# Performance work log

Measured on AMD Instinct MI355X. Metric: run time of the kernel, lower is better.

The kernel has to match this reference:

```python
import jax, jax.numpy as jnp
import numpy as np

HID = 192
EPS = 1e-5

def _bn(x, g, b):
    # BatchNorm1d, training mode: batch stats over all leading axes, biased var
    ax = tuple(range(x.ndim - 1))
    m = x.mean(axis=ax)
    v = x.var(axis=ax)
    return (x - m) * jax.lax.rsqrt(v + EPS) * g + b

def _glorot(k, shape):
    lim = np.sqrt(6.0 / (shape[0] + shape[1]))
    return jax.random.uniform(k, shape, jnp.float32, -lim, lim)

def setup_inputs() -> dict:
    key = jax.random.key(0)
    ks = jax.random.split(key, 8)
    B, N, F, C = 16, 1024, 128, 10
    x = jax.random.normal(ks[0], (B, N, F), jnp.float32)
    adj = (jax.random.uniform(ks[1], (B, N, N)) < 0.01).astype(jnp.float32)
    adj = jnp.maximum(adj, jnp.swapaxes(adj, 1, 2))
    return dict(
        x=x, adj=adj,
        bn_feat_g=jnp.ones((F,), jnp.float32), bn_feat_b=jnp.full((F,), 1e-4, jnp.float32),
        W_feat=_glorot(ks[2], (F, HID)),
        bns_conv_g=jnp.ones((3, HID), jnp.float32), bns_conv_b=jnp.full((3, HID), 1e-4, jnp.float32),
        convs_W=jnp.stack([_glorot(jax.random.fold_in(ks[3], i), (HID, HID)) for i in range(3)]),
        convs_b=jnp.zeros((3, HID), jnp.float32),
        bn_fc_g=jnp.ones((HID,), jnp.float32), bn_fc_b=jnp.full((HID,), 1e-4, jnp.float32),
        lin_W=_glorot(ks[4], (HID, HID)), lin_b=jnp.zeros((HID,), jnp.float32),
        bn_hid_g=jnp.ones((HID,), jnp.float32), bn_hid_b=jnp.full((HID,), 1e-4, jnp.float32),
        cls_W=_glorot(ks[5], (HID, 10)), cls_b=jnp.zeros((10,), jnp.float32),
    )

def reference(x, adj, bn_feat_g, bn_feat_b, W_feat, bns_conv_g, bns_conv_b,
              convs_W, convs_b, bn_fc_g, bn_fc_b, lin_W, lin_b,
              bn_hid_g, bn_hid_b, cls_W, cls_b):
    B, N, _ = x.shape
    # dense_to_sparse discards edge values -> binary edges; add remaining self loops (weight 1)
    A = (adj != 0).astype(x.dtype)
    A = jnp.maximum(A, jnp.eye(N, dtype=x.dtype))
    deg = A.sum(-1)                                   # [B,N]
    dis = jnp.where(deg > 0, deg ** -0.5, 0.0)
    A_hat = dis[:, :, None] * A * dis[:, None, :]      # D^-1/2 (A+I) D^-1/2
    h = _bn(x, bn_feat_g, bn_feat_b)
    # conv_feat has gfn=True: pure linear transform, no bias, no propagation
    h = jax.nn.relu(jnp.einsum('bnf,fh->bnh', h, W_feat))
    for i in range(convs_W.shape[0]):
        h = _bn(h, bns_conv_g[i], bns_conv_b[i])
        h = jax.nn.relu(jnp.einsum('bij,bjh->bih', A_hat, h @ convs_W[i]) + convs_b[i])
    g = h.mean(axis=1)                                 # global_mean_pool -> [B,HID]
    g = _bn(g, bn_fc_g, bn_fc_b)
    g = jax.nn.relu(g @ lin_W + lin_b)
    g = _bn(g, bn_hid_g, bn_hid_b)
    logits = g @ cls_W + cls_b
    return jax.nn.log_softmax(logits, axis=-1)
```

## Files before the change

### kernel.cpp

```cpp
#include <hip/hip_runtime.h>
#include <hip/hip_bf16.h>

#define BB 16
#define NN 1024
#define FF 128
#define HH 192
#define NROWS (BB*NN)
#define MAXC 128
#define EPSV 1e-5f

constexpr size_t OFF_H0  = 0;
constexpr size_t OFF_ZB  = OFF_H0 + (size_t)NROWS*HH/2;
constexpr size_t OFF_WPF = OFF_ZB + (size_t)NROWS*HH/2;
constexpr size_t OFF_WPC = OFF_WPF + (size_t)HH*FF/2;
constexpr size_t OFF_BF  = OFF_WPC + (size_t)HH*HH/2;
constexpr size_t OFF_BC  = OFF_BF + HH;
constexpr size_t OFF_DIS = OFF_BC + HH;
constexpr size_t OFF_G   = OFF_DIS + NROWS;
constexpr size_t OFF_ST  = OFF_G + BB*HH;
constexpr size_t ST_SIZE = 512 + 3*8*512;
constexpr size_t OFF_FLAG= OFF_ST + ST_SIZE;
constexpr size_t OFF_CNT = OFF_FLAG + 1;
constexpr size_t OFF_COLS= OFF_CNT + NROWS;

typedef __attribute__((ext_vector_type(8))) short short8;
typedef __attribute__((ext_vector_type(4))) float f32x4;
typedef __attribute__((ext_vector_type(4))) unsigned int u32x4;
typedef __attribute__((ext_vector_type(2))) unsigned int u32x2;

static __device__ __forceinline__ float bf(const __hip_bfloat16 v) {
    return __bfloat162float(v);
}
static __device__ __forceinline__ float ldin(const void* p, size_t i, int isf) {
    return isf ? ((const float*)p)[i]
               : __bfloat162float(((const __hip_bfloat16*)p)[i]);
}
static __host__ __device__ __forceinline__ float* stage_h(float* ws, int s ) {
    return ws + OFF_ST + 512 + (size_t)s*8*512;
}

__global__ void detect_and_zero(const unsigned int* __restrict__ adjw, float* ws) {
    __shared__ int evid;
    int tid = threadIdx.x;
    if (tid == 0) evid = 0;
    __syncthreads();
    int local = 0;
    for (int k = tid; k < 16384; k += 256) {
        unsigned int w = adjw[k];
        if ((w & 0xFFFFu) == 0x3F80u) local++;
    }
    if (local) atomicAdd(&evid, local);
    for (size_t k = tid; k < ST_SIZE; k += 256) ws[OFF_ST + k] = 0.f;
    for (int k = tid; k < BB*HH; k += 256) ws[OFF_G + k] = 0.f;
    __syncthreads();
    if (tid == 0) ((int*)ws)[OFF_FLAG] = (evid == 0) ? 1 : 0;
}

__global__ __launch_bounds__(256) void phase1(const void* __restrict__ adj,
                                              const void* __restrict__ x, float* ws) {
    const int isf = ((const int*)ws)[OFF_FLAG];
    int tid = threadIdx.x;
    if (blockIdx.x < NROWS) {
        int row = blockIdx.x;
        int i   = row & (NN - 1);
        __shared__ int cnt_s;
        __shared__ unsigned short colbuf[MAXC];
        if (tid == 0) cnt_s = 0;
        __syncthreads();
        int j0 = tid*4;
        unsigned int bits[4];
        if (isf) {
            u32x4 v = *(const u32x4*)((const unsigned int*)adj + (size_t)row*NN + j0);
            bits[0]=v[0]; bits[1]=v[1]; bits[2]=v[2]; bits[3]=v[3];
        } else {
            u32x2 v = *(const u32x2*)((const unsigned short*)adj + (size_t)row*NN + j0);
            bits[0]=(v[0]&0xFFFFu); bits[1]=(v[0]>>16); bits[2]=(v[1]&0xFFFFu); bits[3]=(v[1]>>16);
        }
        #pragma unroll
        for (int e = 0; e < 4; ++e) {
            int j = j0 + e;
            if ((bits[e] << 1) != 0u || j == i) {
                int p = atomicAdd(&cnt_s, 1);
                if (p < MAXC) colbuf[p] = (unsigned short)j;
            }
        }
        __syncthreads();
        int c = cnt_s; if (c > MAXC) c = MAXC;
        if (tid == 0) {
            ((int*)(ws + OFF_CNT))[row] = c;
            ws[OFF_DIS + row] = rsqrtf((float)cnt_s);
        }
        unsigned short* cols = (unsigned short*)(ws + OFF_COLS);
        for (int k = tid; k < c; k += 256) cols[(size_t)row*MAXC + k] = colbuf[k];
    } else {
        int b2 = blockIdx.x - NROWS;
        int f = tid & (FF-1), half = tid >> 7;
        int r0 = b2*64 + half*32;
        float s = 0.f, sq = 0.f;
        for (int r = 0; r < 32; ++r) {
            float v = ldin(x, (size_t)(r0 + r)*FF + f, isf);
            s += v; sq += v*v;
        }
        atomicAdd(&ws[OFF_ST + f], s);
        atomicAdd(&ws[OFF_ST + 256 + f], sq);
    }
}

__global__ void prep_feat(const void* __restrict__ W_feat,
                          const void* __restrict__ gg, const void* __restrict__ bb,
                          float* ws) {
    const int isf = ((const int*)ws)[OFF_FLAG];
    int n = blockIdx.x, k = threadIdx.x;
    const float* st = ws + OFF_ST;
    float m   = st[k] * (1.f/NROWS);
    float var = st[256+k] * (1.f/NROWS) - m*m;
    float a   = ldin(gg, k, isf) * rsqrtf(var + EPSV);
    float c   = ldin(bb, k, isf) - m*a;
    float wv  = ldin(W_feat, (size_t)k*HH + n, isf);
    ((__hip_bfloat16*)(ws + OFF_WPF))[(size_t)n*FF + k] = __float2bfloat16(a*wv);
    __shared__ float red[FF];
    red[k] = c*wv;
    __syncthreads();
    for (int s = FF/2; s > 0; s >>= 1) {
        if (k < s) red[k] += red[k + s];
        __syncthreads();
    }
    if (k == 0) ws[OFF_BF + n] = red[0];
}

__global__ void prep_conv(const void* __restrict__ convs_W,
                          const void* __restrict__ gg, const void* __restrict__ bb,
                          int layer, float* ws) {
    const int isf = ((const int*)ws)[OFF_FLAG];
    int n = blockIdx.x, k = threadIdx.x;
    const float* st = stage_h(ws, layer);
    float s = 0.f, sq = 0.f;
    #pragma unroll
    for (int bkt = 0; bkt < 8; ++bkt) {
        s  += st[bkt*512 + k];
        sq += st[bkt*512 + 256 + k];
    }
    float m   = s * (1.f/NROWS);
    float var = sq * (1.f/NROWS) - m*m;
    float a   = ldin(gg, (size_t)layer*HH + k, isf) * rsqrtf(var + EPSV);
    float c   = ldin(bb, (size_t)layer*HH + k, isf) - m*a;
    float wv  = ldin(convs_W, (size_t)layer*HH*HH + (size_t)k*HH + n, isf);
    ((__hip_bfloat16*)(ws + OFF_WPC))[(size_t)n*HH + k] = __float2bfloat16(a*wv);
    __shared__ float red[HH];
    red[k] = c*wv;
    __syncthreads();
    if (k < 96) red[k] += red[k + 96];
    __syncthreads();
    for (int s2 = 48; s2 >= 3; s2 >>= 1) {
        if (k < s2) red[k] += red[k + s2];
        __syncthreads();
    }
    if (k == 0) ws[OFF_BC + n] = red[0] + red[1] + red[2];
}

template<int K, int MODE>
__global__ __launch_bounds__(256) void gemm_mfma(const void* __restrict__ A,
                                                 const __hip_bfloat16* __restrict__ BT,
                                                 const float* __restrict__ bias,
                                                 float* __restrict__ ws) {
    const int isf = ((const int*)ws)[OFF_FLAG];
    int lane = threadIdx.x & 63, w = threadIdx.x >> 6;
    int wr = w & 1, wc = w >> 1;
    int row0 = blockIdx.x*32 + wr*16;
    int col0 = wc*96;
    int m    = lane & 15, quad = lane >> 4;
    f32x4 acc[6];
    #pragma unroll
    for (int t = 0; t < 6; ++t) acc[t] = f32x4{0.f,0.f,0.f,0.f};
    float bv[6];
    #pragma unroll
    for (int t = 0; t < 6; ++t) bv[t] = bias[col0 + t*16 + m];
    #pragma unroll
    for (int kb = 0; kb < K/32; ++kb) {
        short8 a;
        if (MODE == 0 && isf) {
            const float* Ar = (const float*)A + (size_t)(row0+m)*K + kb*32 + quad*8;
            f32x4 v0 = *(const f32x4*)Ar;
            f32x4 v1 = *(const f32x4*)(Ar + 4);
            union { short8 s8; __hip_bfloat16 h[8]; } u;
            #pragma unroll
            for (int e = 0; e < 4; ++e) {
                u.h[e]   = __float2bfloat16(v0[e]);
                u.h[e+4] = __float2bfloat16(v1[e]);
            }
            a = u.s8;
        } else {
            a = *(const short8*)((const __hip_bfloat16*)A +
                                 (size_t)(row0+m)*K + kb*32 + quad*8);
        }
        #pragma unroll
        for (int t = 0; t < 6; ++t) {
            short8 b = *(const short8*)(BT + (size_t)(col0 + t*16+m)*K + kb*32 + quad*8);
            acc[t] = __builtin_amdgcn_mfma_f32_16x16x32_bf16(a, b, acc[t], 0, 0, 0);
        }
    }
    if (MODE == 0) {
        __shared__ float sh[2*HH];
        for (int i = threadIdx.x; i < 2*HH; i += 256) sh[i] = 0.f;
        __syncthreads();
        __hip_bfloat16* H0 = (__hip_bfloat16*)(ws + OFF_H0);
        #pragma unroll
        for (int t = 0; t < 6; ++t) {
            int ch = col0 + t*16 + m;
            float s = 0.f, sq = 0.f;
            #pragma unroll
            for (int r = 0; r < 4; ++r) {
                float o = fmaxf(acc[t][r] + bv[t], 0.f);
                H0[(size_t)(row0 + quad*4 + r)*HH + ch] = __float2bfloat16(o);
                s += o; sq += o*o;
            }
            atomicAdd(&sh[ch], s);
            atomicAdd(&sh[HH + ch], sq);
        }
        __syncthreads();
        float* st = stage_h(ws, 0) + (blockIdx.x & 7)*512;
        if (threadIdx.x < HH) {
            atomicAdd(&st[threadIdx.x], sh[threadIdx.x]);
            atomicAdd(&st[256 + threadIdx.x], sh[HH + threadIdx.x]);
        }
    } else {
        const float* dis = ws + OFF_DIS;
        __hip_bfloat16* Z = (__hip_bfloat16*)(ws + OFF_ZB);
        float sc[4];
        #pragma unroll
        for (int r = 0; r < 4; ++r) sc[r] = dis[row0 + quad*4 + r];
        #pragma unroll
        for (int t = 0; t < 6; ++t)
            #pragma unroll
            for (int r = 0; r < 4; ++r)
                Z[(size_t)(row0 + quad*4 + r)*HH + col0 + t*16 + m] =
                    __float2bfloat16((acc[t][r] + bv[t]) * sc[r]);
    }
}

__global__ __launch_bounds__(192) void spmm(const void* __restrict__ bias, int layer,
                                            float* __restrict__ stat_out, int is_pool,
                                            float* ws) {
    int tid = threadIdx.x;
    const int isf = ((const int*)ws)[OFF_FLAG];
    const float* dis = ws + OFF_DIS;
    const int* cnt = (const int*)(ws + OFF_CNT);
    const unsigned short* cols = (const unsigned short*)(ws + OFF_COLS);
    const __hip_bfloat16* Z = (const __hip_bfloat16*)(ws + OFF_ZB);
    __hip_bfloat16* H0 = (__hip_bfloat16*)(ws + OFF_H0);
    int r0 = blockIdx.x * 4;
    int base = (r0 >> 10) << 10;
    float bl = ldin(bias, (size_t)layer*HH + tid, isf);
    float s = 0.f, sq = 0.f;
    #pragma unroll
    for (int rr = 0; rr < 4; ++rr) {
        int row = r0 + rr;
        int c = cnt[row];
        const unsigned short* cl = cols + (size_t)row*MAXC;
        float acc = 0.f;
        int k = 0;
        for (; k + 4 <= c; k += 4) {
            int j0 = base + cl[k],   j1 = base + cl[k+1];
            int j2 = base + cl[k+2], j3 = base + cl[k+3];
            acc += bf(Z[(size_t)j0*HH + tid]) + bf(Z[(size_t)j1*HH + tid])
                 + bf(Z[(size_t)j2*HH + tid]) + bf(Z[(size_t)j3*HH + tid]);
        }
        for (; k < c; ++k) acc += bf(Z[(size_t)(base + cl[k])*HH + tid]);
        float o = fmaxf(dis[row]*acc + bl, 0.f);
        H0[(size_t)row*HH + tid] = __float2bfloat16(o);
        s += o; sq += o*o;
    }
    if (is_pool) {
        atomicAdd(&ws[OFF_G + (size_t)(r0 >> 10)*HH + tid], s);
    } else {
        float* st = stat_out + (blockIdx.x & 7)*512;
        atomicAdd(&st[tid], s);
        atomicAdd(&st[256 + tid], sq);
    }
}

__global__ __launch_bounds__(768) void tail(
                     const void* __restrict__ fc_g,  const void* __restrict__ fc_b,
                     const void* __restrict__ lin_W, const void* __restrict__ lin_b,
                     const void* __restrict__ hid_g, const void* __restrict__ hid_b,
                     const void* __restrict__ cls_W, const void* __restrict__ cls_b,
                     void* __restrict__ out, const float* ws) {
    __shared__ float g1[BB][HH];
    __shared__ float g2[BB][HH];
    __shared__ __hip_bfloat16 Wl[HH*HH];
    __shared__ float logits[BB][10];
    __shared__ float lse[BB];
    int tid = threadIdx.x;
    const int isf = ((const int*)ws)[OFF_FLAG];
    const float* g = ws + OFF_G;
    if (isf) {
        const float* Wp = (const float*)lin_W;
        for (int i = tid; i < HH*HH; i += 768) Wl[i] = __float2bfloat16(Wp[i]);
    } else {
        const __hip_bfloat16* Wp = (const __hip_bfloat16*)lin_W;
        for (int i = tid; i < HH*HH; i += 768) Wl[i] = Wp[i];
    }
    if (tid < HH) {
        float s = 0.f, sq = 0.f;
        for (int b = 0; b < BB; ++b) {
            float v = g[b*HH + tid] * (1.f/NN);
            s += v; sq += v*v;
        }
        float m = s*(1.f/BB), var = sq*(1.f/BB) - m*m;
        float a = ldin(fc_g, tid, isf) * rsqrtf(var + EPSV);
        float c = ldin(fc_b, tid, isf) - m*a;
        for (int b = 0; b < BB; ++b) g1[b][tid] = g[b*HH + tid]*(1.f/NN)*a + c;
    }
    __syncthreads();
    {
        int n = tid % HH, bg = tid / HH;
        float lb = ldin(lin_b, n, isf);
        float a0 = lb, a1 = lb, a2 = lb, a3 = lb;
        int b0 = bg*4;
        for (int k = 0; k < HH; ++k) {
            float wv = bf(Wl[k*HH + n]);
            a0 += g1[b0+0][k]*wv;
            a1 += g1[b0+1][k]*wv;
            a2 += g1[b0+2][k]*wv;
            a3 += g1[b0+3][k]*wv;
        }
        g2[b0+0][n] = fmaxf(a0, 0.f);
        g2[b0+1][n] = fmaxf(a1, 0.f);
        g2[b0+2][n] = fmaxf(a2, 0.f);
        g2[b0+3][n] = fmaxf(a3, 0.f);
    }
    __syncthreads();
    if (tid < HH) {
        float s = 0.f, sq = 0.f;
        for (int b = 0; b < BB; ++b) { float v = g2[b][tid]; s += v; sq += v*v; }
        float m = s*(1.f/BB), var = sq*(1.f/BB) - m*m;
        float a = ldin(hid_g, tid, isf) * rsqrtf(var + EPSV);
        float c = ldin(hid_b, tid, isf) - m*a;
        for (int b = 0; b < BB; ++b) g2[b][tid] = g2[b][tid]*a + c;
    }
    __syncthreads();
    if (tid < BB*10) {
        int b = tid/10, k = tid%10;
        float acc = ldin(cls_b, k, isf);
        for (int h = 0; h < HH; ++h) acc += g2[b][h] * ldin(cls_W, (size_t)h*10 + k, isf);
        logits[b][k] = acc;
    }
    __syncthreads();
    if (tid < BB) {
        float m = -1e30f;
        for (int k = 0; k < 10; ++k) m = fmaxf(m, logits[tid][k]);
        float s = 0.f;
        for (int k = 0; k < 10; ++k) s += expf(logits[tid][k] - m);
        lse[tid] = m + logf(s);
    }
    __syncthreads();
    if (tid < BB*10) {
        int b = tid/10;
        float v = logits[b][tid%10] - lse[b];
        if (isf) ((float*)out)[tid] = v;
        else     ((__hip_bfloat16*)out)[tid] = __float2bfloat16(v);
    }
}

extern "C" void kernel_launch(void* const* d_in, const int* in_sizes, int n_in,
                              void* d_out, int out_size, void* d_ws, size_t ws_size,
                              hipStream_t stream) {
    const void* x       = d_in[0];
    const void* adj     = d_in[1];
    const void* bnf_g   = d_in[2];
    const void* bnf_b   = d_in[3];
    const void* W_feat  = d_in[4];
    const void* bnc_g   = d_in[5];
    const void* bnc_b   = d_in[6];
    const void* convs_W = d_in[7];
    const void* convs_b = d_in[8];
    const void* fc_g    = d_in[9];
    const void* fc_b    = d_in[10];
    const void* lin_W   = d_in[11];
    const void* lin_b   = d_in[12];
    const void* hid_g   = d_in[13];
    const void* hid_b   = d_in[14];
    const void* cls_W   = d_in[15];
    const void* cls_b   = d_in[16];

    float* ws = (float*)d_ws;
    const __hip_bfloat16* WPF = (const __hip_bfloat16*)(ws + OFF_WPF);
    const __hip_bfloat16* WPC = (const __hip_bfloat16*)(ws + OFF_WPC);

    detect_and_zero<<<1, 256, 0, stream>>>((const unsigned int*)adj, ws);
    phase1<<<NROWS + 256, 256, 0, stream>>>(adj, x, ws);
    prep_feat<<<HH, FF, 0, stream>>>(W_feat, bnf_g, bnf_b, ws);
    gemm_mfma<FF, 0><<<NROWS/32, 256, 0, stream>>>(x, WPF, ws + OFF_BF, ws);
    for (int l = 0; l < 3; ++l) {
        prep_conv<<<HH, HH, 0, stream>>>(convs_W, bnc_g, bnc_b, l, ws);
        gemm_mfma<HH, 1><<<NROWS/32, 256, 0, stream>>>(
            (const void*)(ws + OFF_H0), WPC, ws + OFF_BC, ws);
        spmm<<<NROWS/4, HH, 0, stream>>>(convs_b, l,
            (l < 2) ? stage_h(ws, l + 1) : nullptr, (l == 2) ? 1 : 0, ws);
    }
    tail<<<1, 768, 0, stream>>>(fc_g, fc_b, lin_W, lin_b,
                                hid_g, hid_b, cls_W, cls_b, d_out, ws);
}
```

Before: 387.1 us.

## Restructure SpMM to process rows in parallel with packed bf16 loads

The SpMM kernel now assigns 96 threads per row, with each thread loading two packed bf16 channels as one 32-bit word. Four rows are handled concurrently per block instead of sequentially. Column indices are read eight at a time with a vector load, and per-block statistics are reduced through shared-memory atomics before the global atomics. Block indices in both the GEMM and SpMM kernels are interleaved across batches so that concurrently running blocks touch different graphs. This trades sequential per-row loops for more memory-level parallelism, at the cost of a block-wide sync and extra shared atomics.

```diff
diff --git a/kernel.cpp b/kernel.cpp
--- a/kernel.cpp
+++ b/kernel.cpp
@@ -38,6 +38,17 @@
 static __host__ __device__ __forceinline__ float* stage_h(float* ws, int s ) {
     return ws + OFF_ST + 512 + (size_t)s*8*512;
 }
+static __device__ __forceinline__ float blo(unsigned int u) {
+    union { unsigned int x; float f; } v; v.x = u << 16; return v.f;
+}
+static __device__ __forceinline__ float bhi(unsigned int u) {
+    union { unsigned int x; float f; } v; v.x = u & 0xFFFF0000u; return v.f;
+}
+static __device__ __forceinline__ unsigned int packbf(float a, float b) {
+    union { unsigned int u; __hip_bfloat16 h[2]; } p;
+    p.h[0] = __float2bfloat16(a); p.h[1] = __float2bfloat16(b);
+    return p.u;
+}
 
 __global__ void detect_and_zero(const unsigned int* __restrict__ adjw, float* ws) {
     __shared__ int evid;
@@ -166,7 +177,9 @@
     const int isf = ((const int*)ws)[OFF_FLAG];
     int lane = threadIdx.x & 63, w = threadIdx.x >> 6;
     int wr = w & 1, wc = w >> 1;
-    int row0 = blockIdx.x*32 + wr*16;
+    int bi = blockIdx.x;
+    int batch = bi & 15, seg = bi >> 4;
+    int row0 = batch*NN + seg*32 + wr*16;
     int col0 = wc*96;
     int m    = lane & 15, quad = lane >> 4;
     f32x4 acc[6];
@@ -218,7 +231,7 @@
             atomicAdd(&sh[HH + ch], sq);
         }
         __syncthreads();
-        float* st = stage_h(ws, 0) + (blockIdx.x & 7)*512;
+        float* st = stage_h(ws, 0) + (bi & 7)*512;
         if (threadIdx.x < HH) {
             atomicAdd(&st[threadIdx.x], sh[threadIdx.x]);
             atomicAdd(&st[256 + threadIdx.x], sh[HH + threadIdx.x]);
@@ -238,44 +251,71 @@
     }
 }
 
-__global__ __launch_bounds__(192) void spmm(const void* __restrict__ bias, int layer,
+__global__ __launch_bounds__(384) void spmm(const void* __restrict__ bias, int layer,
                                             float* __restrict__ stat_out, int is_pool,
                                             float* ws) {
     int tid = threadIdx.x;
-    const int isf = ((const int*)ws)[OFF_FLAG];
+    int rl  = tid / 96;
+    int t   = tid - rl*96;
+    const int isf = ((const int*)ws)[OFF_FLAG];
+    int bi = blockIdx.x;
+    int batch = bi & 15, seg = bi >> 4;
+    int row  = batch*NN + seg*4 + rl;
+    int base = batch*NN;
     const float* dis = ws + OFF_DIS;
-    const int* cnt = (const int*)(ws + OFF_CNT);
-    const unsigned short* cols = (const unsigned short*)(ws + OFF_COLS);
-    const __hip_bfloat16* Z = (const __hip_bfloat16*)(ws + OFF_ZB);
-    __hip_bfloat16* H0 = (__hip_bfloat16*)(ws + OFF_H0);
-    int r0 = blockIdx.x * 4;
-    int base = (r0 >> 10) << 10;
-    float bl = ldin(bias, (size_t)layer*HH + tid, isf);
-    float s = 0.f, sq = 0.f;
-    #pragma unroll
-    for (int rr = 0; rr < 4; ++rr) {
-        int row = r0 + rr;
-        int c = cnt[row];
-        const unsigned short* cl = cols + (size_t)row*MAXC;
-        float acc = 0.f;
-        int k = 0;
-        for (; k + 4 <= c; k += 4) {
-            int j0 = base + cl[k],   j1 = base + cl[k+1];
-            int j2 = base + cl[k+2], j3 = base + cl[k+3];
-            acc += bf(Z[(size_t)j0*HH + tid]) + bf(Z[(size_t)j1*HH + tid])
-                 + bf(Z[(size_t)j2*HH + tid]) + bf(Z[(size_t)j3*HH + tid]);
-        }
-        for (; k < c; ++k) acc += bf(Z[(size_t)(base + cl[k])*HH + tid]);
-        float o = fmaxf(dis[row]*acc + bl, 0.f);
-        H0[(size_t)row*HH + tid] = __float2bfloat16(o);
-        s += o; sq += o*o;
-    }
+    int c = ((const int*)(ws + OFF_CNT))[row];
+    const unsigned short* cl = (const unsigned short*)(ws + OFF_COLS) + (size_t)row*MAXC;
+    const unsigned int* Zu = (const unsigned int*)(ws + OFF_ZB);
+    __shared__ float sh_s[HH];
+    __shared__ float sh_q[HH];
+    if (!is_pool) {
+        for (int i = tid; i < HH; i += 384) { sh_s[i] = 0.f; sh_q[i] = 0.f; }
+    } else {
+        for (int i = tid; i < HH; i += 384) sh_s[i] = 0.f;
+    }
+    __syncthreads();
+    float a0 = 0.f, a1 = 0.f;
+    int k = 0;
+    for (; k + 8 <= c; k += 8) {
+        u32x4 cw = *(const u32x4*)(cl + k);
+        int j[8];
+        j[0] = (int)(cw[0] & 0xFFFFu); j[1] = (int)(cw[0] >> 16);
+        j[2] = (int)(cw[1] & 0xFFFFu); j[3] = (int)(cw[1] >> 16);
+        j[4] = (int)(cw[2] & 0xFFFFu); j[5] = (int)(cw[2] >> 16);
+        j[6] = (int)(cw[3] & 0xFFFFu); j[7] = (int)(cw[3] >> 16);
+        unsigned int z[8];
+        #pragma unroll
+        for (int e = 0; e < 8; ++e)
+            z[e] = Zu[(size_t)(base + j[e])*96 + t];
+        #pragma unroll
+        for (int e = 0; e < 8; ++e) { a0 += blo(z[e]); a1 += bhi(z[e]); }
+    }
+    for (; k < c; ++k) {
+        unsigned int z = Zu[(size_t)(base + (int)cl[k])*96 + t];
+        a0 += blo(z); a1 += bhi(z);
+    }
+    float d  = dis[row];
+    float b0 = ldin(bias, (size_t)layer*HH + 2*t,     isf);
+    float b1 = ldin(bias, (size_t)layer*HH + 2*t + 1, isf);
+    float o0 = fmaxf(d*a0 + b0, 0.f);
+    float o1 = fmaxf(d*a1 + b1, 0.f);
+    ((unsigned int*)(ws + OFF_H0))[(size_t)row*96 + t] = packbf(o0, o1);
     if (is_pool) {
-        atomicAdd(&ws[OFF_G + (size_t)(r0 >> 10)*HH + tid], s);
+        atomicAdd(&sh_s[2*t],     o0);
+        atomicAdd(&sh_s[2*t + 1], o1);
+        __syncthreads();
+        if (tid < HH) atomicAdd(&ws[OFF_G + (size_t)batch*HH + tid], sh_s[tid]);
     } else {
-        float* st = stat_out + (blockIdx.x & 7)*512;
-        atomicAdd(&st[tid], s);
-        atomicAdd(&st[256 + tid], sq);
+        atomicAdd(&sh_s[2*t],     o0);
+        atomicAdd(&sh_s[2*t + 1], o1);
+        atomicAdd(&sh_q[2*t],     o0*o0);
+        atomicAdd(&sh_q[2*t + 1], o1*o1);
+        __syncthreads();
+        float* st = stat_out + (bi & 7)*512;
+        if (tid < HH) {
+            atomicAdd(&st[tid],       sh_s[tid]);
+            atomicAdd(&st[256 + tid], sh_q[tid]);
+        }
     }
 }
 
@@ -395,7 +435,7 @@
         prep_conv<<<HH, HH, 0, stream>>>(convs_W, bnc_g, bnc_b, l, ws);
         gemm_mfma<HH, 1><<<NROWS/32, 256, 0, stream>>>(
             (const void*)(ws + OFF_H0), WPC, ws + OFF_BC, ws);
-        spmm<<<NROWS/4, HH, 0, stream>>>(convs_b, l,
+        spmm<<<NROWS/4, 384, 0, stream>>>(convs_b, l,
             (l < 2) ? stage_h(ws, l + 1) : nullptr, (l == 2) ? 1 : 0, ws);
     }
     tail<<<1, 768, 0, stream>>>(fc_g, fc_b, lin_W, lin_b,
```

Result: faster. 356.3 us (-8.0%).
